# Kernel optimization log

Hardware: AMD Instinct MI355X
Metric: run time of the kernel (lower is better)

Reference implementation:

```python
import jax, jax.numpy as jnp
import numpy as np

L, H, DH, D, F, BLK, VOCAB = 2, 16, 128, 2048, 8192, 64, 32000
B, S, R = 16, 77, 16
LORA_SCALE = 32.0 / 16.0  # alpha / r

# standard bitsandbytes NF4 codebook
NF4 = jnp.array([-1.0, -0.6961928009986877, -0.5250730514526367,
                 -0.39491748809814453, -0.28444138169288635, -0.18477343022823334,
                 -0.09105003625154495, 0.0, 0.07958029955625534, 0.16093020141124725,
                 0.24611230194568634, 0.33791524171829224, 0.44070982933044434,
                 0.5626170039176941, 0.723855197429657, 1.0], dtype=jnp.float32)


def setup_inputs() -> dict:
    key = jax.random.key(0)
    ks = jax.random.split(key, 24)
    n = lambda k, sh, s=0.02: jax.random.normal(k, sh, jnp.float32) * s
    u = lambda k, sh: jax.random.uniform(k, sh, dtype=jnp.float32) * 0.02
    ri = lambda k, sh, hi: jax.random.randint(k, sh, 0, hi, jnp.int32)
    return {
        "input_ids": ri(ks[0], (B, S), VOCAB),
        "attention_mask": jnp.ones((B, S), jnp.int32),
        "embed": n(ks[1], (VOCAB, D)),
        "ln_attn": jnp.ones((L, D), jnp.float32),
        "ln_mlp": jnp.ones((L, D), jnp.float32),
        "ln_final": jnp.ones((D,), jnp.float32),
        "qkv_codes": ri(ks[2], (L, 3, D, D), 16),
        "qkv_absmax": u(ks[3], (L, 3, D, D // BLK)),
        "qkv_A": n(ks[4], (L, 3, R, D)),
        "qkv_B": n(ks[5], (L, 3, D, R), 0.01),
        "o_codes": ri(ks[6], (L, D, D), 16),
        "o_absmax": u(ks[7], (L, D, D // BLK)),
        "o_A": n(ks[8], (L, R, D)),
        "o_B": n(ks[9], (L, D, R), 0.01),
        "gu_codes": ri(ks[10], (L, 2, F, D), 16),
        "gu_absmax": u(ks[11], (L, 2, F, D // BLK)),
        "gu_A": n(ks[12], (L, 2, R, D)),
        "gu_B": n(ks[13], (L, 2, F, R), 0.01),
        "down_codes": ri(ks[14], (L, D, F), 16),
        "down_absmax": u(ks[15], (L, D, F // BLK)),
        "down_A": n(ks[16], (L, R, F)),
        "down_B": n(ks[17], (L, D, R), 0.01),
    }


def _rmsnorm(x, w, eps=1e-6):
    return x * jax.lax.rsqrt(jnp.mean(x * x, axis=-1, keepdims=True) + eps) * w


def _dequant(codes, absmax):
    # codes: (out, cin) ints in [0,16); absmax: (out, cin//BLK) blockwise scales
    out, cin = codes.shape
    w = NF4[codes].reshape(out, cin // BLK, BLK) * absmax[..., None]
    return w.reshape(out, cin)


def _qlora(x, codes, absmax, A, Bm):
    # NF4 dequant base matmul + rank-R LoRA delta (eval mode, no dropout)
    W = _dequant(codes, absmax)
    return x @ W.T + LORA_SCALE * ((x @ A.T) @ Bm.T)


def _rope_cache(seq):
    inv = 1.0 / (10000.0 ** (jnp.arange(0, DH, 2, dtype=jnp.float32) / DH))
    f = jnp.arange(seq, dtype=jnp.float32)[:, None] * inv  # (S, DH/2)
    emb = jnp.concatenate([f, f], axis=-1)                 # (S, DH)
    return jnp.cos(emb), jnp.sin(emb)


def _rope(x, cos, sin):
    # x: (B, H, S, DH), llama-style rotate_half
    x1, x2 = jnp.split(x, 2, axis=-1)
    return x * cos + jnp.concatenate([-x2, x1], axis=-1) * sin


def _forward(input_ids, attention_mask, embed, ln_attn, ln_mlp, ln_final,
             qkv_codes, qkv_absmax, qkv_A, qkv_B,
             o_codes, o_absmax, o_A, o_B,
             gu_codes, gu_absmax, gu_A, gu_B,
             down_codes, down_absmax, down_A, down_B):
    b, s = input_ids.shape
    h = embed[input_ids]                                    # (B, S, D)
    cos, sin = _rope_cache(s)
    pad = attention_mask.astype(bool)[:, None, None, :]     # (B,1,1,S)
    mask = pad & jnp.tril(jnp.ones((s, s), bool))
    inv_sqrt_dh = np.float32(1.0 / np.sqrt(DH))
    for l in range(L):
        x = _rmsnorm(h, ln_attn[l])
        q, k, v = [_qlora(x, qkv_codes[l, i], qkv_absmax[l, i], qkv_A[l, i], qkv_B[l, i])
                   .reshape(b, s, H, DH).transpose(0, 2, 1, 3) for i in range(3)]
        q, k = _rope(q, cos, sin), _rope(k, cos, sin)
        scores = jnp.einsum('bhqd,bhkd->bhqk', q, k) * inv_sqrt_dh
        attn = jax.nn.softmax(jnp.where(mask, scores, -1e9), axis=-1)
        o = jnp.einsum('bhqk,bhkd->bhqd', attn, v).transpose(0, 2, 1, 3).reshape(b, s, D)
        h = h + _qlora(o, o_codes[l], o_absmax[l], o_A[l], o_B[l])
        x = _rmsnorm(h, ln_mlp[l])
        g = _qlora(x, gu_codes[l, 0], gu_absmax[l, 0], gu_A[l, 0], gu_B[l, 0])
        up = _qlora(x, gu_codes[l, 1], gu_absmax[l, 1], gu_A[l, 1], gu_B[l, 1])
        h = h + _qlora(jax.nn.silu(g) * up,
                       down_codes[l], down_absmax[l], down_A[l], down_B[l])
    h = _rmsnorm(h, ln_final)
    lengths = attention_mask.sum(axis=1) - 1                # last non-pad token index
    return h[jnp.arange(b), lengths]                        # (B, D)


def reference(input_ids, attention_mask, embed, ln_attn, ln_mlp, ln_final,
              qkv_codes, qkv_absmax, qkv_A, qkv_B,
              o_codes, o_absmax, o_A, o_B,
              gu_codes, gu_absmax, gu_A, gu_B,
              down_codes, down_absmax, down_A, down_B):
    return _forward(input_ids, attention_mask, embed, ln_attn, ln_mlp, ln_final,
                    qkv_codes, qkv_absmax, qkv_A, qkv_B,
                    o_codes, o_absmax, o_A, o_B,
                    gu_codes, gu_absmax, gu_A, gu_B,
                    down_codes, down_absmax, down_A, down_B)
```

## Files before the change

### kernel.cpp

```cpp
#include <hip/hip_runtime.h>
#include <cstdint>
#include <cstddef>

#define M_TOK   1232
#define M_PAD   1280
#define D_MODEL 2048
#define F_FFN   8192
#define SEQ     77
#define BATCH   16
#define NHEAD   16
#define LRANK   16
#define NLAYER  2
#define ATILE   16

typedef short bf16x8 __attribute__((ext_vector_type(8)));
typedef float f32x4  __attribute__((ext_vector_type(4)));

__device__ __constant__ float NF4C[16] = {
  -1.0f, -0.6961928009986877f, -0.5250730514526367f, -0.39491748809814453f,
  -0.28444138169288635f, -0.18477343022823334f, -0.09105003625154495f, 0.0f,
  0.07958029955625534f, 0.16093020141124725f, 0.24611230194568634f,
  0.33791524171829224f, 0.44070982933044434f, 0.5626170039176941f,
  0.723855197429657f, 1.0f };

__device__ inline unsigned short f2b(float f) {
  unsigned u = __builtin_bit_cast(unsigned, f);
  u += 0x7FFFu + ((u >> 16) & 1u);
  return (unsigned short)(u >> 16);
}
__device__ inline float b2f(unsigned short s) {
  return __builtin_bit_cast(float, ((unsigned)s) << 16);
}

__global__ __launch_bounds__(256) void mat_w(
    const int* __restrict__ C, const float* __restrict__ AM,
    unsigned short* __restrict__ W, int K, long total8)
{
  __shared__ float tb[16];
  if (threadIdx.x < 16) tb[threadIdx.x] = NF4C[threadIdx.x];
  __syncthreads();
  const int KB = K >> 6;
  for (long i = (long)blockIdx.x * 256 + threadIdx.x; i < total8;
       i += (long)gridDim.x * 256) {
    long e = i << 3;
    int n = (int)(e / K), k = (int)(e - (long)n * K);
    float am = AM[(size_t)n * KB + (k >> 6)];
    const int4* cp = (const int4*)(C + e);
    int4 a = cp[0], b = cp[1];
    uint4 o;
    o.x = (unsigned)f2b(tb[a.x] * am) | ((unsigned)f2b(tb[a.y] * am) << 16);
    o.y = (unsigned)f2b(tb[a.z] * am) | ((unsigned)f2b(tb[a.w] * am) << 16);
    o.z = (unsigned)f2b(tb[b.x] * am) | ((unsigned)f2b(tb[b.y] * am) << 16);
    o.w = (unsigned)f2b(tb[b.z] * am) | ((unsigned)f2b(tb[b.w] * am) << 16);
    *(uint4*)(W + e) = o;
  }
}

__global__ __launch_bounds__(256, 2) void gemm_bf(
    const unsigned short* __restrict__ X, const unsigned short* __restrict__ W,
    float* __restrict__ O, int mb, int N, int K, int acc_mode, int splitk,
    const float* __restrict__ T, const float* __restrict__ Bm, int sh, int nr)
{
  __shared__ __align__(16) unsigned short xs[128 * 64];
  __shared__ __align__(16) unsigned short ws[128 * 64];

  int tid = threadIdx.x;

  int nwg = gridDim.x;
  int q8 = nwg >> 3, r8 = nwg & 7;
  int xcd = blockIdx.x & 7, pos = blockIdx.x >> 3;
  int wgid = (xcd < r8) ? (xcd * (q8 + 1) + pos)
                        : (r8 * (q8 + 1) + (xcd - r8) * q8 + pos);
  int nb = N >> 7;
  int per = mb * nb;
  int slice = wgid / per; int rem = wgid - slice * per;
  int nblk = rem / mb, mblk = rem - nblk * mb;
  int row0 = mblk << 7, col0 = nblk << 7;
  int KBtot = K >> 6, kcnt = KBtot / splitk, kbeg = slice * kcnt;

  int wave = tid >> 6, lane = tid & 63;
  int fr = lane & 15, fg = lane >> 4, s7 = fr & 7;
  int wm = (wave >> 1) * 64, wn = (wave & 1) * 64;
  int xg = lane >> 3;
  int xcol = (((lane & 7) ^ (xg & 7)) << 3);

  const unsigned short* Xbase = X + (size_t)row0 * K + (size_t)kbeg * 64;
  const unsigned short* Wbase = W + (size_t)col0 * K + (size_t)kbeg * 64;

  f32x4 accm[4][4];
  #pragma unroll
  for (int i = 0; i < 4; ++i)
    #pragma unroll
    for (int j = 0; j < 4; ++j) accm[i][j] = (f32x4){0.f, 0.f, 0.f, 0.f};

  auto stage = [&](int t) {
    const unsigned short* xb = Xbase + (size_t)t * 64;
    const unsigned short* wb = Wbase + (size_t)t * 64;
    #pragma unroll
    for (int p2 = 0; p2 < 4; ++p2) {
      int c = wave * 4 + p2;
      const unsigned short* gp = xb + (size_t)(c * 8 + xg) * K + xcol;
      __builtin_amdgcn_global_load_lds(
          (const __attribute__((address_space(1))) unsigned int*)gp,
          (__attribute__((address_space(3))) unsigned int*)(xs + c * 512),
          16, 0, 0);
    }
    #pragma unroll
    for (int p2 = 0; p2 < 4; ++p2) {
      int c = wave * 4 + p2;
      const unsigned short* gp = wb + (size_t)(c * 8 + xg) * K + xcol;
      __builtin_amdgcn_global_load_lds(
          (const __attribute__((address_space(1))) unsigned int*)gp,
          (__attribute__((address_space(3))) unsigned int*)(ws + c * 512),
          16, 0, 0);
    }
  };
  auto compute = [&]() {
    bf16x8 b0[4], b1[4];
    #pragma unroll
    for (int ni = 0; ni < 4; ++ni) {
      const unsigned short* wr = ws + (wn + ni * 16 + fr) * 64;
      b0[ni] = *(const bf16x8*)(wr + ((fg ^ s7) << 3));
      b1[ni] = *(const bf16x8*)(wr + (((4 | fg) ^ s7) << 3));
    }
    #pragma unroll
    for (int mi = 0; mi < 4; ++mi) {
      const unsigned short* xr = xs + (wm + mi * 16 + fr) * 64;
      bf16x8 a0 = *(const bf16x8*)(xr + ((fg ^ s7) << 3));
      bf16x8 a1 = *(const bf16x8*)(xr + (((4 | fg) ^ s7) << 3));
      #pragma unroll
      for (int ni = 0; ni < 4; ++ni) {
        accm[mi][ni] = __builtin_amdgcn_mfma_f32_16x16x32_bf16(
            a0, b0[ni], accm[mi][ni], 0, 0, 0);
        accm[mi][ni] = __builtin_amdgcn_mfma_f32_16x16x32_bf16(
            a1, b1[ni], accm[mi][ni], 0, 0, 0);
      }
    }
  };

  stage(0);
  for (int t = 0; t < kcnt; ++t) {
    __syncthreads();
    compute();
    if (t + 1 < kcnt) {
      __syncthreads();
      stage(t + 1);
    }
  }

  float* Tt = (float*)&xs[0];
  float* Bt = (float*)&ws[0];
  if (T) {
    __syncthreads();
    int toff = (col0 >> sh) << 4;
    for (int idx = tid; idx < 128 * 16; idx += 256) {
      int rr = idx >> 4, c = idx & 15;
      int gm = row0 + rr;
      Tt[idx] = (gm < M_TOK) ? T[(size_t)gm * nr + toff + c] : 0.f;
      Bt[idx] = Bm[(size_t)(col0 + rr) * LRANK + c];
    }
    __syncthreads();
  }

  #pragma unroll
  for (int mi = 0; mi < 4; ++mi)
    #pragma unroll
    for (int ni = 0; ni < 4; ++ni) {
      int gm0 = row0 + wm + mi * 16 + fg * 4;
      int gnl = wn + ni * 16 + fr;
      int gn = col0 + gnl;
      #pragma unroll
      for (int r = 0; r < 4; ++r) {
        int gm = gm0 + r;
        if (gm < M_TOK) {
          size_t idx = (size_t)gm * N + gn;
          float vv = accm[mi][ni][r];
          if (T) {
            const float* tr = Tt + (wm + mi * 16 + fg * 4 + r) * 16;
            const float* br = Bt + gnl * 16;
            float s = 0.f;
            #pragma unroll
            for (int c = 0; c < 16; ++c) s += tr[c] * br[c];
            vv += 2.0f * s;
          }
          if (splitk > 1)       atomicAdd(&O[idx], vv);
          else if (acc_mode)    O[idx] += vv;
          else                  O[idx] = vv;
        }
      }
    }
}

__global__ __launch_bounds__(256) void lora1(
    const unsigned short* __restrict__ X, const float* __restrict__ A,
    float* __restrict__ T, int K)
{
  int m0 = blockIdx.x * 4, bi = blockIdx.y, nmat = gridDim.y;
  int g = threadIdx.x >> 4, l16 = threadIdx.x & 15;
  const float* ar = A + (size_t)bi * LRANK * K + (size_t)g * K;
  const unsigned short* x0 = X + (size_t)m0 * K;
  float s0 = 0.f, s1 = 0.f, s2 = 0.f, s3 = 0.f;
  for (int kk = l16 * 4; kk < K; kk += 64) {
    float4 av = *(const float4*)(ar + kk);
    ushort4 v0 = *(const ushort4*)(x0 + kk);
    ushort4 v1 = *(const ushort4*)(x0 + K + kk);
    ushort4 v2 = *(const ushort4*)(x0 + 2 * K + kk);
    ushort4 v3 = *(const ushort4*)(x0 + 3 * K + kk);
    s0 += b2f(v0.x)*av.x + b2f(v0.y)*av.y + b2f(v0.z)*av.z + b2f(v0.w)*av.w;
    s1 += b2f(v1.x)*av.x + b2f(v1.y)*av.y + b2f(v1.z)*av.z + b2f(v1.w)*av.w;
    s2 += b2f(v2.x)*av.x + b2f(v2.y)*av.y + b2f(v2.z)*av.z + b2f(v2.w)*av.w;
    s3 += b2f(v3.x)*av.x + b2f(v3.y)*av.y + b2f(v3.z)*av.z + b2f(v3.w)*av.w;
  }
  #pragma unroll
  for (int off = 8; off; off >>= 1) {
    s0 += __shfl_down(s0, off, 16);
    s1 += __shfl_down(s1, off, 16);
    s2 += __shfl_down(s2, off, 16);
    s3 += __shfl_down(s3, off, 16);
  }
  if (l16 == 0) {
    size_t base = ((size_t)m0 * nmat + bi) * LRANK + g;
    size_t rs = (size_t)nmat * LRANK;
    T[base] = s0; T[base + rs] = s1; T[base + 2*rs] = s2; T[base + 3*rs] = s3;
  }
}

__global__ __launch_bounds__(256) void lora2(
    float* __restrict__ O, const float* __restrict__ T,
    const float* __restrict__ Bm, int N, int sh, int nr)
{
  int m0 = blockIdx.y * 8;
  int n = blockIdx.x * 256 + threadIdx.x;
  __shared__ float ts[8 * 48];
  for (int i = threadIdx.x; i < 8 * nr; i += 256)
    ts[(i / nr) * 48 + (i % nr)] = T[(size_t)(m0 + i / nr) * nr + (i % nr)];
  __syncthreads();
  const float4* br = (const float4*)(Bm + (size_t)n * LRANK);
  float4 b0 = br[0], b1 = br[1], b2 = br[2], b3 = br[3];
  int toff = ((n >> sh) << 4);
  #pragma unroll
  for (int mi = 0; mi < 8; ++mi) {
    const float* tsb = ts + mi * 48 + toff;
    float s = b0.x*tsb[0] + b0.y*tsb[1] + b0.z*tsb[2] + b0.w*tsb[3]
            + b1.x*tsb[4] + b1.y*tsb[5] + b1.z*tsb[6] + b1.w*tsb[7]
            + b2.x*tsb[8] + b2.y*tsb[9] + b2.z*tsb[10] + b2.w*tsb[11]
            + b3.x*tsb[12] + b3.y*tsb[13] + b3.z*tsb[14] + b3.w*tsb[15];
    O[(size_t)(m0 + mi) * N + n] += 2.0f * s;
  }
}

__global__ __launch_bounds__(256) void rmsnorm_k(
    const float* __restrict__ H, const float* __restrict__ W,
    unsigned short* __restrict__ X, int D)
{
  int m = blockIdx.x;
  const float* hr = H + (size_t)m * D;
  float s = 0.f;
  for (int i = threadIdx.x; i < D; i += 256) { float v = hr[i]; s += v * v; }
  __shared__ float red[4];
  #pragma unroll
  for (int off = 32; off; off >>= 1) s += __shfl_down(s, off, 64);
  if ((threadIdx.x & 63) == 0) red[threadIdx.x >> 6] = s;
  __syncthreads();
  float tot = red[0] + red[1] + red[2] + red[3];
  float inv = rsqrtf(tot / (float)D + 1e-6f);
  for (int i = threadIdx.x; i < D; i += 256)
    X[(size_t)m * D + i] = f2b(hr[i] * inv * W[i]);
}

__global__ void rope_table(float* __restrict__ cosT, float* __restrict__ sinT)
{
  int idx = blockIdx.x * 64 + threadIdx.x;
  if (idx >= SEQ * 64) return;
  int s = idx >> 6, j = idx & 63;
  float inv = powf(10000.0f, -(float)(2 * j) / 128.0f);
  float f = (float)s * inv;
  cosT[idx] = cosf(f);
  sinT[idx] = sinf(f);
}

__global__ void rope_apply(float* __restrict__ QKV,
                           const float* __restrict__ cosT, const float* __restrict__ sinT)
{
  size_t idx = (size_t)blockIdx.x * 256 + threadIdx.x;
  if (idx >= (size_t)M_TOK * NHEAD * 64) return;
  int j = (int)(idx & 63);
  int h = (int)((idx >> 6) & (NHEAD - 1));
  int m = (int)(idx >> 10);
  int s = m % SEQ;
  float c = cosT[s * 64 + j], sn = sinT[s * 64 + j];
  size_t base = (size_t)m * (3 * D_MODEL) + h * 128;
  float q1 = QKV[base + j], q2 = QKV[base + 64 + j];
  QKV[base + j]      = q1 * c - q2 * sn;
  QKV[base + 64 + j] = q2 * c + q1 * sn;
  size_t kb = base + D_MODEL;
  float k1 = QKV[kb + j], k2 = QKV[kb + 64 + j];
  QKV[kb + j]      = k1 * c - k2 * sn;
  QKV[kb + 64 + j] = k2 * c + k1 * sn;
}

__global__ __launch_bounds__(256) void attn_k(
    const float* __restrict__ QKV, const int* __restrict__ amask,
    unsigned short* __restrict__ O)
{
  int bh = blockIdx.x, it = blockIdx.y;
  int b = bh >> 4, h = bh & (NHEAD - 1);
  const int STR = 3 * D_MODEL;
  __shared__ float ks[SEQ * 132];
  __shared__ float sc[ATILE * 80];
  __shared__ int am[SEQ];
  const float scale = 0.08838834764831845f;

  const float* Kbase = QKV + (size_t)(b * SEQ) * STR + D_MODEL + h * 128;
  for (int idx = threadIdx.x; idx < SEQ * 32; idx += 256) {
    int j = idx >> 5, d4 = (idx & 31) << 2;
    *(float4*)(ks + j * 132 + d4) = *(const float4*)(Kbase + (size_t)j * STR + d4);
  }
  for (int j = threadIdx.x; j < SEQ; j += 256) am[j] = amask[b * SEQ + j];
  __syncthreads();

  int wave = threadIdx.x >> 6, lane = threadIdx.x & 63;
  #pragma unroll
  for (int r = 0; r < 4; ++r) {
    int il = wave * 4 + r;
    int i = it * ATILE + il;
    if (i < SEQ) {
      const float4* qr = (const float4*)(QKV + (size_t)(b * SEQ + i) * STR + h * 128);
      int j1 = lane, j2 = lane + 64;
      float v1 = -1e9f, v2 = -1e9f;
      if (j1 <= i && am[j1]) {
        const float4* kr = (const float4*)(ks + j1 * 132);
        float s = 0.f;
        #pragma unroll 8
        for (int d = 0; d < 32; ++d) {
          float4 a = qr[d], c = kr[d];
          s += a.x*c.x + a.y*c.y + a.z*c.z + a.w*c.w;
        }
        v1 = s * scale;
      }
      if (j2 < SEQ && j2 <= i && am[j2]) {
        const float4* kr = (const float4*)(ks + j2 * 132);
        float s = 0.f;
        #pragma unroll 8
        for (int d = 0; d < 32; ++d) {
          float4 a = qr[d], c = kr[d];
          s += a.x*c.x + a.y*c.y + a.z*c.z + a.w*c.w;
        }
        v2 = s * scale;
      }
      float mx = fmaxf(v1, v2);
      #pragma unroll
      for (int off = 32; off; off >>= 1) mx = fmaxf(mx, __shfl_xor(mx, off));
      float e1 = __expf(v1 - mx);
      float e2 = (j2 < SEQ) ? __expf(v2 - mx) : 0.f;
      float sum = e1 + e2;
      #pragma unroll
      for (int off = 32; off; off >>= 1) sum += __shfl_xor(sum, off);
      float inv = 1.0f / sum;
      sc[il * 80 + j1] = e1 * inv;
      if (j2 < SEQ) sc[il * 80 + j2] = e2 * inv;
    }
  }
  __syncthreads();

  const float* Vbase = QKV + (size_t)(b * SEQ) * STR + 2 * D_MODEL + h * 128;
  for (int idx = threadIdx.x; idx < ATILE * 32; idx += 256) {
    int il = idx >> 5, d4 = (idx & 31) << 2;
    int i = it * ATILE + il;
    if (i >= SEQ) continue;
    float4 acc = {0.f, 0.f, 0.f, 0.f};
    const float* sr = sc + il * 80;
    for (int j = 0; j < SEQ; ++j) {
      float pp = sr[j];
      float4 v = *(const float4*)(Vbase + (size_t)j * STR + d4);
      acc.x += pp * v.x; acc.y += pp * v.y; acc.z += pp * v.z; acc.w += pp * v.w;
    }
    unsigned short* op = O + (size_t)(b * SEQ + i) * D_MODEL + h * 128 + d4;
    op[0] = f2b(acc.x); op[1] = f2b(acc.y); op[2] = f2b(acc.z); op[3] = f2b(acc.w);
  }
}

__global__ void embed_gather(const float* __restrict__ E, const int* __restrict__ ids,
                             float* __restrict__ H)
{
  size_t idx = (size_t)blockIdx.x * 256 + threadIdx.x;
  int m = (int)(idx / D_MODEL);
  int n = (int)(idx % D_MODEL);
  H[idx] = E[(size_t)ids[m] * D_MODEL + n];
}

__global__ void silu_mul(const float* __restrict__ GU, unsigned short* __restrict__ GB)
{
  size_t id = (size_t)blockIdx.x * 256 + threadIdx.x;
  int m = (int)(id >> 13), n = (int)(id & (F_FFN - 1));
  float g = GU[(size_t)m * 2 * F_FFN + n];
  float u = GU[(size_t)m * 2 * F_FFN + F_FFN + n];
  float sig = 1.0f / (1.0f + expf(-g));
  GB[id] = f2b(g * sig * u);
}

__global__ __launch_bounds__(256) void final_k(
    const float* __restrict__ H, const int* __restrict__ amask,
    const float* __restrict__ W, float* __restrict__ out)
{
  int b = blockIdx.x;
  __shared__ int len;
  if (threadIdx.x == 0) {
    int s = 0;
    for (int j = 0; j < SEQ; ++j) s += amask[b * SEQ + j];
    len = s - 1;
  }
  __syncthreads();
  const float* hr = H + ((size_t)(b * SEQ + len) * D_MODEL);
  float s = 0.f;
  for (int i = threadIdx.x; i < D_MODEL; i += 256) { float v = hr[i]; s += v * v; }
  __shared__ float red[4];
  #pragma unroll
  for (int off = 32; off; off >>= 1) s += __shfl_down(s, off, 64);
  if ((threadIdx.x & 63) == 0) red[threadIdx.x >> 6] = s;
  __syncthreads();
  float tot = red[0] + red[1] + red[2] + red[3];
  float inv = rsqrtf(tot / (float)D_MODEL + 1e-6f);
  for (int i = threadIdx.x; i < D_MODEL; i += 256)
    out[(size_t)b * D_MODEL + i] = hr[i] * inv * W[i];
}

extern "C" void kernel_launch(void* const* d_in, const int* in_sizes, int n_in,
                              void* d_out, int out_size, void* d_ws, size_t ws_size,
                              hipStream_t stream) {
  const int*   ids     = (const int*)d_in[0];
  const int*   amask   = (const int*)d_in[1];
  const float* embed   = (const float*)d_in[2];
  const float* ln_attn = (const float*)d_in[3];
  const float* ln_mlp  = (const float*)d_in[4];
  const float* ln_fin  = (const float*)d_in[5];
  const int*   qkvC    = (const int*)d_in[6];
  const float* qkvS    = (const float*)d_in[7];
  const float* qkvA    = (const float*)d_in[8];
  const float* qkvB    = (const float*)d_in[9];
  const int*   oC      = (const int*)d_in[10];
  const float* oS      = (const float*)d_in[11];
  const float* oA      = (const float*)d_in[12];
  const float* oB      = (const float*)d_in[13];
  const int*   guC     = (const int*)d_in[14];
  const float* guS     = (const float*)d_in[15];
  const float* guA     = (const float*)d_in[16];
  const float* guB     = (const float*)d_in[17];
  const int*   dnC     = (const int*)d_in[18];
  const float* dnS     = (const float*)d_in[19];
  const float* dnA     = (const float*)d_in[20];
  const float* dnB     = (const float*)d_in[21];
  float* out = (float*)d_out;

  const int M = M_TOK, Mp = M_PAD, D = D_MODEL, F = F_FFN, R = LRANK;
  float* p = (float*)d_ws;
  float* h    = p; p += (size_t)Mp * D;
  float* qkv  = p; p += (size_t)Mp * 3 * D;
  float* gu   = p; p += (size_t)Mp * 2 * F;
  float* t    = p; p += (size_t)Mp * 48;
  float* cosT = p; p += SEQ * 64;
  float* sinT = p; p += SEQ * 64;
  unsigned short* xbf = (unsigned short*)p; p += (size_t)Mp * D / 2;
  unsigned short* gbf = (unsigned short*)qkv;
  unsigned short* wbuf = (unsigned short*)p;
  p += (size_t)2 * F * D / 2;

  rope_table<<<(SEQ*64 + 63)/64, 64, 0, stream>>>(cosT, sinT);
  embed_gather<<<(M * D)/256, 256, 0, stream>>>(embed, ids, h);

  const int mb = Mp / 128;

  for (int l = 0; l < NLAYER; ++l) {
    rmsnorm_k<<<M, 256, 0, stream>>>(h, ln_attn + (size_t)l * D, xbf, D);
    lora1<<<dim3(M/4, 3), 256, 0, stream>>>(xbf, qkvA + (size_t)l*3*R*D, t, D);
    mat_w<<<4096, 256, 0, stream>>>(qkvC + (size_t)l*3*D*D, qkvS + (size_t)l*3*D*(D/64),
                                    wbuf, D, (long)3*D*D/8);
    gemm_bf<<<mb * (3*D/128), 256, 0, stream>>>(
        xbf, wbuf, qkv, mb, 3*D, D, 0, 1,
        t, qkvB + (size_t)l*3*D*R, 11, 48);
    rope_apply<<<((size_t)M*NHEAD*64 + 255)/256, 256, 0, stream>>>(qkv, cosT, sinT);
    attn_k<<<dim3(BATCH*NHEAD, (SEQ + ATILE - 1)/ATILE), 256, 0, stream>>>(qkv, amask, xbf);
    mat_w<<<2048, 256, 0, stream>>>(oC + (size_t)l*D*D, oS + (size_t)l*D*(D/64),
                                    wbuf, D, (long)D*D/8);
    gemm_bf<<<mb * (D/128) * 8, 256, 0, stream>>>(
        xbf, wbuf, h, mb, D, D, 1, 8, nullptr, nullptr, 0, 0);
    lora1<<<dim3(M/4, 1), 256, 0, stream>>>(xbf, oA + (size_t)l*R*D, t, D);
    lora2<<<dim3(D/256, M/8), 256, 0, stream>>>(h, t, oB + (size_t)l*D*R, D, 11, 16);

    rmsnorm_k<<<M, 256, 0, stream>>>(h, ln_mlp + (size_t)l * D, xbf, D);
    lora1<<<dim3(M/4, 2), 256, 0, stream>>>(xbf, guA + (size_t)l*2*R*D, t, D);
    mat_w<<<4096, 256, 0, stream>>>(guC + (size_t)l*2*F*D, guS + (size_t)l*2*F*(D/64),
                                    wbuf, D, (long)2*F*D/8);
    gemm_bf<<<mb * (2*F/128), 256, 0, stream>>>(
        xbf, wbuf, gu, mb, 2*F, D, 0, 1,
        t, guB + (size_t)l*2*F*R, 13, 32);
    silu_mul<<<((size_t)M * F)/256, 256, 0, stream>>>(gu, gbf);
    mat_w<<<4096, 256, 0, stream>>>(dnC + (size_t)l*D*F, dnS + (size_t)l*D*(F/64),
                                    wbuf, F, (long)D*F/8);
    gemm_bf<<<mb * (D/128) * 8, 256, 0, stream>>>(
        gbf, wbuf, h, mb, D, F, 1, 8, nullptr, nullptr, 0, 0);
    lora1<<<dim3(M/4, 1), 256, 0, stream>>>(gbf, dnA + (size_t)l*R*F, t, F);
    lora2<<<dim3(D/256, M/8), 256, 0, stream>>>(h, t, dnB + (size_t)l*D*R, D, 11, 16);
  }
  final_k<<<BATCH, 256, 0, stream>>>(h, amask, ln_fin, out);
}
```

Before: 1.336 ms.

## Fuse SiLU-gate into gate/up GEMM via interleaved weights, fold RoPE into attention

The gate/up dequantized weight rows are interleaved so that each GEMM tile holds matching gate and up columns. The epilogue adds the LoRA term, pairs neighbouring lanes with a shuffle, and writes silu(g)*up straight to bf16. This removes the fp32 gate/up intermediate and the separate silu_mul kernel. RoPE is now applied while Q/K are loaded into shared memory in the attention kernel, which drops the rope_apply pass, and the o-projection split-K goes from 8 to 4. The cost is a strided-row gather in mat_w and a heavier GEMM epilogue with per-element rank-16 dot products.

```diff
diff --git a/kernel.cpp b/kernel.cpp
--- a/kernel.cpp
+++ b/kernel.cpp
@@ -34,7 +34,7 @@
 
 __global__ __launch_bounds__(256) void mat_w(
     const int* __restrict__ C, const float* __restrict__ AM,
-    unsigned short* __restrict__ W, int K, long total8)
+    unsigned short* __restrict__ W, int K, long total8, int ilv)
 {
   __shared__ float tb[16];
   if (threadIdx.x < 16) tb[threadIdx.x] = NF4C[threadIdx.x];
@@ -43,9 +43,10 @@
   for (long i = (long)blockIdx.x * 256 + threadIdx.x; i < total8;
        i += (long)gridDim.x * 256) {
     long e = i << 3;
-    int n = (int)(e / K), k = (int)(e - (long)n * K);
-    float am = AM[(size_t)n * KB + (k >> 6)];
-    const int4* cp = (const int4*)(C + e);
+    int rd = (int)(e / K), k = (int)(e - (long)rd * K);
+    int srcn = ilv ? ((rd & 1) * F_FFN + (rd >> 1)) : rd;
+    float am = AM[(size_t)srcn * KB + (k >> 6)];
+    const int4* cp = (const int4*)(C + (size_t)srcn * K + k);
     int4 a = cp[0], b = cp[1];
     uint4 o;
     o.x = (unsigned)f2b(tb[a.x] * am) | ((unsigned)f2b(tb[a.y] * am) << 16);
@@ -59,7 +60,8 @@
 __global__ __launch_bounds__(256, 2) void gemm_bf(
     const unsigned short* __restrict__ X, const unsigned short* __restrict__ W,
     float* __restrict__ O, int mb, int N, int K, int acc_mode, int splitk,
-    const float* __restrict__ T, const float* __restrict__ Bm, int sh, int nr)
+    const float* __restrict__ T, const float* __restrict__ Bm, int sh, int nr,
+    int gum, unsigned short* __restrict__ GB)
 {
   __shared__ __align__(16) unsigned short xs[128 * 64];
   __shared__ __align__(16) unsigned short ws[128 * 64];
@@ -146,6 +148,47 @@
       __syncthreads();
       stage(t + 1);
     }
+  }
+
+  if (gum) {
+    float* Tt = (float*)&xs[0];
+    float* Bt = (float*)&ws[0];
+    __syncthreads();
+    for (int idx = tid; idx < 128 * 32; idx += 256) {
+      int rr = idx >> 5, c = idx & 31;
+      int gm = row0 + rr;
+      Tt[idx] = (gm < M_TOK) ? T[(size_t)gm * 32 + c] : 0.f;
+    }
+    for (int idx = tid; idx < 128 * 16; idx += 256) {
+      int rr = idx >> 4, c = idx & 15;
+      int type = rr & 1, nrow = (col0 + rr) >> 1;
+      Bt[idx] = Bm[((size_t)type * F_FFN + nrow) * LRANK + c];
+    }
+    __syncthreads();
+    #pragma unroll
+    for (int mi = 0; mi < 4; ++mi)
+      #pragma unroll
+      for (int ni = 0; ni < 4; ++ni) {
+        int gm0 = row0 + wm + mi * 16 + fg * 4;
+        int gnl = wn + ni * 16 + fr;
+        #pragma unroll
+        for (int r = 0; r < 4; ++r) {
+          int gm = gm0 + r;
+          float vv = accm[mi][ni][r];
+          const float* tr = Tt + (wm + mi * 16 + fg * 4 + r) * 32 + ((gnl & 1) << 4);
+          const float* br = Bt + gnl * 16;
+          float s = 0.f;
+          #pragma unroll
+          for (int c = 0; c < 16; ++c) s += tr[c] * br[c];
+          vv += 2.0f * s;
+          float prt = __shfl_xor(vv, 1);
+          if (gm < M_TOK && !(fr & 1)) {
+            float sig = 1.0f / (1.0f + expf(-vv));
+            GB[(size_t)gm * F_FFN + ((col0 + gnl) >> 1)] = f2b(vv * sig * prt);
+          }
+        }
+      }
+    return;
   }
 
   float* Tt = (float*)&xs[0];
@@ -279,42 +322,48 @@
   sinT[idx] = sinf(f);
 }
 
-__global__ void rope_apply(float* __restrict__ QKV,
-                           const float* __restrict__ cosT, const float* __restrict__ sinT)
-{
-  size_t idx = (size_t)blockIdx.x * 256 + threadIdx.x;
-  if (idx >= (size_t)M_TOK * NHEAD * 64) return;
-  int j = (int)(idx & 63);
-  int h = (int)((idx >> 6) & (NHEAD - 1));
-  int m = (int)(idx >> 10);
-  int s = m % SEQ;
-  float c = cosT[s * 64 + j], sn = sinT[s * 64 + j];
-  size_t base = (size_t)m * (3 * D_MODEL) + h * 128;
-  float q1 = QKV[base + j], q2 = QKV[base + 64 + j];
-  QKV[base + j]      = q1 * c - q2 * sn;
-  QKV[base + 64 + j] = q2 * c + q1 * sn;
-  size_t kb = base + D_MODEL;
-  float k1 = QKV[kb + j], k2 = QKV[kb + 64 + j];
-  QKV[kb + j]      = k1 * c - k2 * sn;
-  QKV[kb + 64 + j] = k2 * c + k1 * sn;
-}
-
 __global__ __launch_bounds__(256) void attn_k(
     const float* __restrict__ QKV, const int* __restrict__ amask,
+    const float* __restrict__ cosT, const float* __restrict__ sinT,
     unsigned short* __restrict__ O)
 {
   int bh = blockIdx.x, it = blockIdx.y;
   int b = bh >> 4, h = bh & (NHEAD - 1);
   const int STR = 3 * D_MODEL;
   __shared__ float ks[SEQ * 132];
+  __shared__ float qs[ATILE * 132];
   __shared__ float sc[ATILE * 80];
   __shared__ int am[SEQ];
   const float scale = 0.08838834764831845f;
 
-  const float* Kbase = QKV + (size_t)(b * SEQ) * STR + D_MODEL + h * 128;
-  for (int idx = threadIdx.x; idx < SEQ * 32; idx += 256) {
-    int j = idx >> 5, d4 = (idx & 31) << 2;
-    *(float4*)(ks + j * 132 + d4) = *(const float4*)(Kbase + (size_t)j * STR + d4);
+  const float* Kb = QKV + (size_t)(b * SEQ) * STR + D_MODEL + h * 128;
+  for (int idx = threadIdx.x; idx < SEQ * 16; idx += 256) {
+    int j = idx >> 4, dq = (idx & 15) << 2;
+    float4 a = *(const float4*)(Kb + (size_t)j * STR + dq);
+    float4 bb = *(const float4*)(Kb + (size_t)j * STR + dq + 64);
+    float4 c4 = *(const float4*)(cosT + j * 64 + dq);
+    float4 s4 = *(const float4*)(sinT + j * 64 + dq);
+    float* kr = ks + j * 132 + dq;
+    kr[0] = a.x*c4.x - bb.x*s4.x; kr[1] = a.y*c4.y - bb.y*s4.y;
+    kr[2] = a.z*c4.z - bb.z*s4.z; kr[3] = a.w*c4.w - bb.w*s4.w;
+    kr[64] = bb.x*c4.x + a.x*s4.x; kr[65] = bb.y*c4.y + a.y*s4.y;
+    kr[66] = bb.z*c4.z + a.z*s4.z; kr[67] = bb.w*c4.w + a.w*s4.w;
+  }
+  const float* Qb = QKV + (size_t)(b * SEQ) * STR + h * 128;
+  for (int idx = threadIdx.x; idx < ATILE * 16; idx += 256) {
+    int il = idx >> 4, dq = (idx & 15) << 2;
+    int i = it * ATILE + il;
+    if (i < SEQ) {
+      float4 a = *(const float4*)(Qb + (size_t)i * STR + dq);
+      float4 bb = *(const float4*)(Qb + (size_t)i * STR + dq + 64);
+      float4 c4 = *(const float4*)(cosT + i * 64 + dq);
+      float4 s4 = *(const float4*)(sinT + i * 64 + dq);
+      float* qr = qs + il * 132 + dq;
+      qr[0] = a.x*c4.x - bb.x*s4.x; qr[1] = a.y*c4.y - bb.y*s4.y;
+      qr[2] = a.z*c4.z - bb.z*s4.z; qr[3] = a.w*c4.w - bb.w*s4.w;
+      qr[64] = bb.x*c4.x + a.x*s4.x; qr[65] = bb.y*c4.y + a.y*s4.y;
+      qr[66] = bb.z*c4.z + a.z*s4.z; qr[67] = bb.w*c4.w + a.w*s4.w;
+    }
   }
   for (int j = threadIdx.x; j < SEQ; j += 256) am[j] = amask[b * SEQ + j];
   __syncthreads();
@@ -325,7 +374,7 @@
     int il = wave * 4 + r;
     int i = it * ATILE + il;
     if (i < SEQ) {
-      const float4* qr = (const float4*)(QKV + (size_t)(b * SEQ + i) * STR + h * 128);
+      const float4* qr = (const float4*)(qs + il * 132);
       int j1 = lane, j2 = lane + 64;
       float v1 = -1e9f, v2 = -1e9f;
       if (j1 <= i && am[j1]) {
@@ -389,16 +438,6 @@
   H[idx] = E[(size_t)ids[m] * D_MODEL + n];
 }
 
-__global__ void silu_mul(const float* __restrict__ GU, unsigned short* __restrict__ GB)
-{
-  size_t id = (size_t)blockIdx.x * 256 + threadIdx.x;
-  int m = (int)(id >> 13), n = (int)(id & (F_FFN - 1));
-  float g = GU[(size_t)m * 2 * F_FFN + n];
-  float u = GU[(size_t)m * 2 * F_FFN + F_FFN + n];
-  float sig = 1.0f / (1.0f + expf(-g));
-  GB[id] = f2b(g * sig * u);
-}
-
 __global__ __launch_bounds__(256) void final_k(
     const float* __restrict__ H, const int* __restrict__ amask,
     const float* __restrict__ W, float* __restrict__ out)
@@ -456,12 +495,11 @@
   float* p = (float*)d_ws;
   float* h    = p; p += (size_t)Mp * D;
   float* qkv  = p; p += (size_t)Mp * 3 * D;
-  float* gu   = p; p += (size_t)Mp * 2 * F;
   float* t    = p; p += (size_t)Mp * 48;
   float* cosT = p; p += SEQ * 64;
   float* sinT = p; p += SEQ * 64;
   unsigned short* xbf = (unsigned short*)p; p += (size_t)Mp * D / 2;
-  unsigned short* gbf = (unsigned short*)qkv;
+  unsigned short* gbf = (unsigned short*)p; p += (size_t)Mp * F / 2;
   unsigned short* wbuf = (unsigned short*)p;
   p += (size_t)2 * F * D / 2;
 
@@ -474,31 +512,30 @@
     rmsnorm_k<<<M, 256, 0, stream>>>(h, ln_attn + (size_t)l * D, xbf, D);
     lora1<<<dim3(M/4, 3), 256, 0, stream>>>(xbf, qkvA + (size_t)l*3*R*D, t, D);
     mat_w<<<4096, 256, 0, stream>>>(qkvC + (size_t)l*3*D*D, qkvS + (size_t)l*3*D*(D/64),
-                                    wbuf, D, (long)3*D*D/8);
+                                    wbuf, D, (long)3*D*D/8, 0);
     gemm_bf<<<mb * (3*D/128), 256, 0, stream>>>(
         xbf, wbuf, qkv, mb, 3*D, D, 0, 1,
-        t, qkvB + (size_t)l*3*D*R, 11, 48);
-    rope_apply<<<((size_t)M*NHEAD*64 + 255)/256, 256, 0, stream>>>(qkv, cosT, sinT);
-    attn_k<<<dim3(BATCH*NHEAD, (SEQ + ATILE - 1)/ATILE), 256, 0, stream>>>(qkv, amask, xbf);
+        t, qkvB + (size_t)l*3*D*R, 11, 48, 0, nullptr);
+    attn_k<<<dim3(BATCH*NHEAD, (SEQ + ATILE - 1)/ATILE), 256, 0, stream>>>(
+        qkv, amask, cosT, sinT, xbf);
     mat_w<<<2048, 256, 0, stream>>>(oC + (size_t)l*D*D, oS + (size_t)l*D*(D/64),
-                                    wbuf, D, (long)D*D/8);
-    gemm_bf<<<mb * (D/128) * 8, 256, 0, stream>>>(
-        xbf, wbuf, h, mb, D, D, 1, 8, nullptr, nullptr, 0, 0);
+                                    wbuf, D, (long)D*D/8, 0);
+    gemm_bf<<<mb * (D/128) * 4, 256, 0, stream>>>(
+        xbf, wbuf, h, mb, D, D, 1, 4, nullptr, nullptr, 0, 0, 0, nullptr);
     lora1<<<dim3(M/4, 1), 256, 0, stream>>>(xbf, oA + (size_t)l*R*D, t, D);
     lora2<<<dim3(D/256, M/8), 256, 0, stream>>>(h, t, oB + (size_t)l*D*R, D, 11, 16);
 
     rmsnorm_k<<<M, 256, 0, stream>>>(h, ln_mlp + (size_t)l * D, xbf, D);
     lora1<<<dim3(M/4, 2), 256, 0, stream>>>(xbf, guA + (size_t)l*2*R*D, t, D);
     mat_w<<<4096, 256, 0, stream>>>(guC + (size_t)l*2*F*D, guS + (size_t)l*2*F*(D/64),
-                                    wbuf, D, (long)2*F*D/8);
+                                    wbuf, D, (long)2*F*D/8, 1);
     gemm_bf<<<mb * (2*F/128), 256, 0, stream>>>(
-        xbf, wbuf, gu, mb, 2*F, D, 0, 1,
-        t, guB + (size_t)l*2*F*R, 13, 32);
-    silu_mul<<<((size_t)M * F)/256, 256, 0, stream>>>(gu, gbf);
+        xbf, wbuf, nullptr, mb, 2*F, D, 0, 1,
+        t, guB + (size_t)l*2*F*R, 0, 32, 1, gbf);
     mat_w<<<4096, 256, 0, stream>>>(dnC + (size_t)l*D*F, dnS + (size_t)l*D*(F/64),
-                                    wbuf, F, (long)D*F/8);
+                                    wbuf, F, (long)D*F/8, 0);
     gemm_bf<<<mb * (D/128) * 8, 256, 0, stream>>>(
-        gbf, wbuf, h, mb, D, F, 1, 8, nullptr, nullptr, 0, 0);
+        gbf, wbuf, h, mb, D, F, 1, 8, nullptr, nullptr, 0, 0, 0, nullptr);
     lora1<<<dim3(M/4, 1), 256, 0, stream>>>(gbf, dnA + (size_t)l*R*F, t, F);
     lora2<<<dim3(D/256, M/8), 256, 0, stream>>>(h, t, dnB + (size_t)l*D*R, D, 11, 16);
   }
```

New measurement: 1.234 ms. -7.7%, faster.
